# Kernel optimization log

Measured on AMD Instinct MI355X. Metric: run time of the kernel, lower is better.

## Reference

```python
import jax, jax.numpy as jnp
import numpy as np

B, CIN, H, W = 128, 64, 32, 32
COUT, K, STRIDE, PAD = 64, 3, 1, 1
HO = (H + 2 * PAD - K) // STRIDE + 1
WO = (W + 2 * PAD - K) // STRIDE + 1


def setup_inputs() -> dict:
    key = jax.random.key(0)
    k1, k2 = jax.random.split(key)
    x = jax.random.normal(k1, (B, CIN, H, W), dtype=jnp.float32)
    # weight scaled like torch init: randn / sqrt(k*k*Cin) (orthogonal_ in torch just
    # re-orthogonalizes; scale here matches the fan-in normalization)
    weight = jax.random.normal(k2, (HO, WO, COUT, CIN, K, K), dtype=jnp.float32) / np.sqrt(K * K * CIN)
    bias = jnp.full((COUT, HO, WO), 0.5, dtype=jnp.float32)
    return {"x": x, "weight": weight, "bias": bias}


def reference(x, weight, bias):
    # pad spatial dims
    xp = jnp.pad(x, ((0, 0), (0, 0), (PAD, PAD), (PAD, PAD)))
    # gather row windows: [B, C, Ho, K, Wp]
    ri = (jnp.arange(HO) * STRIDE)[:, None] + jnp.arange(K)[None, :]  # [Ho, K]
    ci = (jnp.arange(WO) * STRIDE)[:, None] + jnp.arange(K)[None, :]  # [Wo, K]
    rows = xp[:, :, ri, :]           # [B, C, Ho, K, Wp]
    patches = rows[:, :, :, :, ci]   # [B, C, Ho, K, Wo, K]
    # per-location matmul: b c h p w q , h w d c p q -> b d h w
    out = jnp.einsum('bchpwq,hwdcpq->bdhw', patches, weight)
    return out + bias[None]
```

## Files before the change

kernel.cpp:

```cpp
#include <hip/hip_runtime.h>
#include <hip/hip_bf16.h>

#define KT 576

typedef __attribute__((ext_vector_type(8))) short  short8;
typedef __attribute__((ext_vector_type(4))) float  f32x4;

#define VMCNT(n) asm volatile("s_waitcnt vmcnt(" #n ")" ::: "memory")
#define SB() __builtin_amdgcn_sched_barrier(0)

__device__ __forceinline__ unsigned short f2bf(float f) {
  union { float f; unsigned int u; } v; v.f = f;
  return (unsigned short)((v.u + 0x7FFFu + ((v.u >> 16) & 1u)) >> 16);
}

__global__ __launch_bounds__(256) void xC2_kernel(const float* __restrict__ x,
                                                  unsigned short* __restrict__ xC2) {
  const int hp = blockIdx.x, bb = blockIdx.y, t = threadIdx.x;
  __shared__ unsigned short tile[32 * 1024];
  const bool interior = (hp >= 1 && hp <= 32);
  if (interior) {
#pragma unroll 4
    for (int i = 0; i < 32; ++i) {
      const int row = i * 32 + (t >> 3);
      const int bl = row >> 6, c = row & 63;
      const int k = t & 7;
      const float4 v = *(const float4*)(x + ((size_t)(bb * 16 + bl) * 64 + c) * 1024 +
                                        (hp - 1) * 32 + k * 4);
      const int base = (k * 4) * 1024 + (c >> 3) * 128 + bl * 8 + (c & 7);
      tile[base]        = f2bf(v.x);
      tile[base + 1024] = f2bf(v.y);
      tile[base + 2048] = f2bf(v.z);
      tile[base + 3072] = f2bf(v.w);
    }
  }
  __syncthreads();
  unsigned short* dst = xC2 + (size_t)hp * 278528 + (size_t)bb * 1024;
  const uint4 z = make_uint4(0u, 0u, 0u, 0u);
  for (int idx = t; idx < 34 * 128; idx += 256) {
    const int wp = idx >> 7, s = idx & 127;
    uint4 v = z;
    if (interior && wp >= 1 && wp <= 32) v = *(const uint4*)&tile[(wp - 1) * 1024 + s * 8];
    *(uint4*)(dst + (size_t)wp * 8192 + s * 8) = v;
  }
}

__global__ __launch_bounds__(256, 1) void lc_main(const float* __restrict__ Wt,
                                                  const float* __restrict__ bias,
                                                  const unsigned short* __restrict__ xC2,
                                                  float* __restrict__ out) {
  __shared__ unsigned short Wl[2][32 * KT];
  __shared__ float blds[128];

  const int bid = (int)blockIdx.x;
  const int swz = (bid & 7) * 64 + (bid >> 3);
  const int h = swz >> 4, rem = swz & 15, wq = rem >> 1, half = rem & 1;
  const int t = threadIdx.x, lane = t & 63, wv = t >> 6;
  const int l15 = lane & 15, lg = lane >> 4;

  if (t < 128)
    blds[t] = bias[(half * 32 + (t & 31)) * 1024 + h * 32 + wq * 4 + (t >> 5)];

  const unsigned short* xA = xC2 + (size_t)wv * 2048 + lg * 128 + l15 * 8;
  const int x7 = l15 & 7;
  const int wrow0 = l15 * KT;
  const int wrow1 = (16 + l15) * KT;

  f32x4 acc[4][2][2];
#pragma unroll
  for (int j = 0; j < 4; ++j)
#pragma unroll
    for (int bt = 0; bt < 2; ++bt)
#pragma unroll
      for (int dt = 0; dt < 2; ++dt) acc[j][bt][dt] = (f32x4){0.f, 0.f, 0.f, 0.f};

  short8 As0[3][3], As1[3][3];
  float4 wreg[18];

#define ISSUE_W(jj)                                                           \
  {                                                                           \
    const float* ws = Wt + (size_t)(h * 32 + wq * 4 + (jj)) * (64 * KT) +     \
                      (size_t)half * (32 * KT);                               \
    _Pragma("unroll")                                                         \
    for (int i = 0; i < 18; ++i) {                                            \
      const float4* p = (const float4*)ws + (i * 256 + t);                    \
      asm volatile("global_load_dwordx4 %0, %1, off" : "=v"(wreg[i]) : "v"(p)); \
    }                                                                         \
  }

#define ISSUE_A(K)                                                            \
  {                                                                           \
    _Pragma("unroll")                                                         \
    for (int s = 0; s < 3; ++s) {                                             \
      const int step = ((K) % 6) * 3 + s;                                     \
      const int pq = step >> 1, p = pq / 3, q = pq - p * 3;                   \
      const size_t off = (size_t)(h + p) * 278528 +                           \
                         (size_t)(wq * 4 + (K) / 6 + q) * 8192 + (step & 1) * 512; \
      const short8* p0 = (const short8*)(xA + off);                           \
      const short8* p1 = (const short8*)(xA + off + 1024);                    \
      asm volatile("global_load_dwordx4 %0, %1, off" : "=v"(As0[(K) % 3][s]) : "v"(p0)); \
      asm volatile("global_load_dwordx4 %0, %1, off" : "=v"(As1[(K) % 3][s]) : "v"(p1)); \
    }                                                                         \
  }

#define SCATTER(buf)                                                          \
  {                                                                           \
    _Pragma("unroll")                                                         \
    for (int i = 0; i < 18; ++i) {                                            \
      const int f = (i * 256 + t) * 4;                                        \
      const int d = (((unsigned)(f >> 6)) * 7282u) >> 16;                     \
      int kn = f - d * 576;                                                   \
      int c = ((unsigned)kn * 7282u) >> 16;                                   \
      int r = kn - c * 9;                                                     \
      const float vv[4] = {wreg[i].x, wreg[i].y, wreg[i].z, wreg[i].w};       \
      _Pragma("unroll")                                                       \
      for (int jx = 0; jx < 4; ++jx) {                                        \
        const int kp = r * 64 + c;                                            \
        const int slot = (kp >> 3) ^ (d & 7);                                 \
        Wl[buf][d * KT + slot * 8 + (kp & 7)] = f2bf(vv[jx]);                 \
        if (++r == 9) { r = 0; ++c; }                                         \
      }                                                                       \
    }                                                                         \
  }

#define STEP(jj, gg, NN)                                                      \
  {                                                                           \
    VMCNT(NN);                                                                \
    SB();                                                                     \
    _Pragma("unroll")                                                         \
    for (int s = 0; s < 3; ++s) {                                             \
      const int sb = ((gg) * 3 + s) * 4 + lg;                                 \
      const short8 b0 = *(const short8*)&Wl[(jj) & 1][wrow0 + ((sb ^ x7) << 3)]; \
      const short8 b1 = *(const short8*)&Wl[(jj) & 1][wrow1 + ((sb ^ x7) << 3)]; \
      acc[(jj)][0][0] = __builtin_amdgcn_mfma_f32_16x16x32_bf16(As0[((jj) * 6 + (gg)) % 3][s], b0, acc[(jj)][0][0], 0, 0, 0); \
      acc[(jj)][1][0] = __builtin_amdgcn_mfma_f32_16x16x32_bf16(As1[((jj) * 6 + (gg)) % 3][s], b0, acc[(jj)][1][0], 0, 0, 0); \
      acc[(jj)][0][1] = __builtin_amdgcn_mfma_f32_16x16x32_bf16(As0[((jj) * 6 + (gg)) % 3][s], b1, acc[(jj)][0][1], 0, 0, 0); \
      acc[(jj)][1][1] = __builtin_amdgcn_mfma_f32_16x16x32_bf16(As1[((jj) * 6 + (gg)) % 3][s], b1, acc[(jj)][1][1], 0, 0, 0); \
    }                                                                         \
  }

  ISSUE_W(0);
  ISSUE_A(0); ISSUE_A(1); ISSUE_A(2);
  VMCNT(18);
  SB();
  SCATTER(0);
  __syncthreads();

  ISSUE_W(1);
  STEP(0, 0, 30); ISSUE_A(3);
  STEP(0, 1, 30); ISSUE_A(4);
  STEP(0, 2, 30); ISSUE_A(5);
  STEP(0, 3, 12); ISSUE_A(6);
  STEP(0, 4, 12); ISSUE_A(7);
  STEP(0, 5, 12); ISSUE_A(8);
  SCATTER(1);
  __syncthreads();

  ISSUE_W(2);
  STEP(1, 0, 30); ISSUE_A(9);
  STEP(1, 1, 30); ISSUE_A(10);
  STEP(1, 2, 30); ISSUE_A(11);
  STEP(1, 3, 12); ISSUE_A(12);
  STEP(1, 4, 12); ISSUE_A(13);
  STEP(1, 5, 12); ISSUE_A(14);
  SCATTER(0);
  __syncthreads();

  ISSUE_W(3);
  STEP(2, 0, 30); ISSUE_A(15);
  STEP(2, 1, 30); ISSUE_A(16);
  STEP(2, 2, 30); ISSUE_A(17);
  STEP(2, 3, 12); ISSUE_A(18);
  STEP(2, 4, 12); ISSUE_A(19);
  STEP(2, 5, 12); ISSUE_A(20);
  SCATTER(1);
  __syncthreads();

  STEP(3, 0, 12); ISSUE_A(21);
  STEP(3, 1, 12); ISSUE_A(22);
  STEP(3, 2, 12); ISSUE_A(23);
  STEP(3, 3, 12);
  STEP(3, 4, 6);
  STEP(3, 5, 0);

#pragma unroll
  for (int dt = 0; dt < 2; ++dt) {
    const int dd = dt * 16 + l15;
    const int dg = half * 32 + dd;
    const float bv0 = blds[dd], bv1 = blds[32 + dd], bv2 = blds[64 + dd], bv3 = blds[96 + dd];
#pragma unroll
    for (int bt = 0; bt < 2; ++bt) {
#pragma unroll
      for (int i = 0; i < 4; ++i) {
        const int b = wv * 32 + bt * 16 + lg * 4 + i;
        float4 v;
        v.x = acc[0][bt][dt][i] + bv0;
        v.y = acc[1][bt][dt][i] + bv1;
        v.z = acc[2][bt][dt][i] + bv2;
        v.w = acc[3][bt][dt][i] + bv3;
        *(float4*)(out + (size_t)b * 65536 + (size_t)dg * 1024 + h * 32 + wq * 4) = v;
      }
    }
  }
}

extern "C" void kernel_launch(void* const* d_in, const int* in_sizes, int n_in,
                              void* d_out, int out_size, void* d_ws, size_t ws_size,
                              hipStream_t stream) {
  const float* x    = (const float*)d_in[0];
  const float* wt   = (const float*)d_in[1];
  const float* bias = (const float*)d_in[2];
  float* out        = (float*)d_out;
  unsigned short* xC2 = (unsigned short*)d_ws;

  xC2_kernel<<<dim3(34, 8), 256, 0, stream>>>(x, xC2);
  lc_main<<<512, 256, 0, stream>>>(wt, bias, xC2, out);
}
```

Measured before the change: 68.54 us.

## Merge output-channel halves into one 512-thread block and split weight staging

Each block now covers all 64 output channels with 8 waves instead of 32 channels with 4 waves. The grid halves from 512 to 256 blocks and weight LDS doubles. The two channel halves share the same activation tiles, which cuts redundant activation fetches. Weight prefetch and scatter are split into two 9-load halves interleaved with the MFMA steps, and wait counts are retuned. With 256 blocks on 256 CUs this risks different occupancy and more LDS pressure per block.

```diff
diff --git a/kernel.cpp b/kernel.cpp
--- a/kernel.cpp
+++ b/kernel.cpp
@@ -45,26 +45,27 @@
   }
 }
 
-__global__ __launch_bounds__(256, 1) void lc_main(const float* __restrict__ Wt,
+__global__ __launch_bounds__(512, 1) void lc_main(const float* __restrict__ Wt,
                                                   const float* __restrict__ bias,
                                                   const unsigned short* __restrict__ xC2,
                                                   float* __restrict__ out) {
-  __shared__ unsigned short Wl[2][32 * KT];
-  __shared__ float blds[128];
+  __shared__ unsigned short Wl[2][64 * KT];
+  __shared__ float blds[256];
 
   const int bid = (int)blockIdx.x;
-  const int swz = (bid & 7) * 64 + (bid >> 3);
-  const int h = swz >> 4, rem = swz & 15, wq = rem >> 1, half = rem & 1;
+  const int swz = (bid & 7) * 32 + (bid >> 3);
+  const int h = swz >> 3, wq = swz & 7;
   const int t = threadIdx.x, lane = t & 63, wv = t >> 6;
+  const int bw = wv & 3, dh = wv >> 2;
   const int l15 = lane & 15, lg = lane >> 4;
 
-  if (t < 128)
-    blds[t] = bias[(half * 32 + (t & 31)) * 1024 + h * 32 + wq * 4 + (t >> 5)];
-
-  const unsigned short* xA = xC2 + (size_t)wv * 2048 + lg * 128 + l15 * 8;
+  if (t < 256)
+    blds[t] = bias[(t & 63) * 1024 + h * 32 + wq * 4 + (t >> 6)];
+
+  const unsigned short* xA = xC2 + (size_t)bw * 2048 + lg * 128 + l15 * 8;
   const int x7 = l15 & 7;
-  const int wrow0 = l15 * KT;
-  const int wrow1 = (16 + l15) * KT;
+  const int wrow0 = (dh * 32 + l15) * KT;
+  const int wrow1 = (dh * 32 + 16 + l15) * KT;
 
   f32x4 acc[4][2][2];
 #pragma unroll
@@ -75,15 +76,15 @@
       for (int dt = 0; dt < 2; ++dt) acc[j][bt][dt] = (f32x4){0.f, 0.f, 0.f, 0.f};
 
   short8 As0[3][3], As1[3][3];
-  float4 wreg[18];
-
-#define ISSUE_W(jj)                                                           \
+  float4 wreg[9];
+
+#define ISSUE_W9(jj, hs)                                                      \
   {                                                                           \
     const float* ws = Wt + (size_t)(h * 32 + wq * 4 + (jj)) * (64 * KT) +     \
-                      (size_t)half * (32 * KT);                               \
-    _Pragma("unroll")                                                         \
-    for (int i = 0; i < 18; ++i) {                                            \
-      const float4* p = (const float4*)ws + (i * 256 + t);                    \
+                      (size_t)(hs) * (32 * KT);                               \
+    _Pragma("unroll")                                                         \
+    for (int i = 0; i < 9; ++i) {                                             \
+      const float4* p = (const float4*)ws + (i * 512 + t);                    \
       asm volatile("global_load_dwordx4 %0, %1, off" : "=v"(wreg[i]) : "v"(p)); \
     }                                                                         \
   }
@@ -103,30 +104,29 @@
     }                                                                         \
   }
 
-#define SCATTER(buf)                                                          \
-  {                                                                           \
-    _Pragma("unroll")                                                         \
-    for (int i = 0; i < 18; ++i) {                                            \
-      const int f = (i * 256 + t) * 4;                                        \
-      const int d = (((unsigned)(f >> 6)) * 7282u) >> 16;                     \
-      int kn = f - d * 576;                                                   \
+#define SCATTER9(buf, hs)                                                     \
+  {                                                                           \
+    _Pragma("unroll")                                                         \
+    for (int i = 0; i < 9; ++i) {                                             \
+      const int f = (i * 512 + t) * 4;                                        \
+      const int dl = (((unsigned)(f >> 6)) * 7282u) >> 16;                    \
+      int kn = f - dl * 576;                                                  \
       int c = ((unsigned)kn * 7282u) >> 16;                                   \
       int r = kn - c * 9;                                                     \
+      const int drow = (hs) * 32 + dl;                                        \
       const float vv[4] = {wreg[i].x, wreg[i].y, wreg[i].z, wreg[i].w};       \
       _Pragma("unroll")                                                       \
       for (int jx = 0; jx < 4; ++jx) {                                        \
         const int kp = r * 64 + c;                                            \
-        const int slot = (kp >> 3) ^ (d & 7);                                 \
-        Wl[buf][d * KT + slot * 8 + (kp & 7)] = f2bf(vv[jx]);                 \
+        const int slot = (kp >> 3) ^ (drow & 7);                              \
+        Wl[buf][drow * KT + slot * 8 + (kp & 7)] = f2bf(vv[jx]);              \
         if (++r == 9) { r = 0; ++c; }                                         \
       }                                                                       \
     }                                                                         \
   }
 
-#define STEP(jj, gg, NN)                                                      \
-  {                                                                           \
-    VMCNT(NN);                                                                \
-    SB();                                                                     \
+#define MFMAS(jj, gg)                                                         \
+  {                                                                           \
     _Pragma("unroll")                                                         \
     for (int s = 0; s < 3; ++s) {                                             \
       const int sb = ((gg) * 3 + s) * 4 + lg;                                 \
@@ -139,42 +139,31 @@
     }                                                                         \
   }
 
-  ISSUE_W(0);
-  ISSUE_A(0); ISSUE_A(1); ISSUE_A(2);
-  VMCNT(18);
-  SB();
-  SCATTER(0);
-  __syncthreads();
-
-  ISSUE_W(1);
-  STEP(0, 0, 30); ISSUE_A(3);
-  STEP(0, 1, 30); ISSUE_A(4);
-  STEP(0, 2, 30); ISSUE_A(5);
-  STEP(0, 3, 12); ISSUE_A(6);
-  STEP(0, 4, 12); ISSUE_A(7);
-  STEP(0, 5, 12); ISSUE_A(8);
-  SCATTER(1);
-  __syncthreads();
-
-  ISSUE_W(2);
-  STEP(1, 0, 30); ISSUE_A(9);
-  STEP(1, 1, 30); ISSUE_A(10);
-  STEP(1, 2, 30); ISSUE_A(11);
-  STEP(1, 3, 12); ISSUE_A(12);
-  STEP(1, 4, 12); ISSUE_A(13);
-  STEP(1, 5, 12); ISSUE_A(14);
-  SCATTER(0);
-  __syncthreads();
-
-  ISSUE_W(3);
-  STEP(2, 0, 30); ISSUE_A(15);
-  STEP(2, 1, 30); ISSUE_A(16);
-  STEP(2, 2, 30); ISSUE_A(17);
-  STEP(2, 3, 12); ISSUE_A(18);
-  STEP(2, 4, 12); ISSUE_A(19);
-  STEP(2, 5, 12); ISSUE_A(20);
-  SCATTER(1);
-  __syncthreads();
+#define STEP(jj, gg, NN) { VMCNT(NN); SB(); MFMAS(jj, gg) }
+
+#define PHASE(jj)                                                             \
+  ISSUE_W9(jj + 1, 0);                                                        \
+  STEP(jj, 0, 21); ISSUE_A(6 * (jj) + 3);                                     \
+  STEP(jj, 1, 21); ISSUE_A(6 * (jj) + 4);                                     \
+  STEP(jj, 2, 21); ISSUE_A(6 * (jj) + 5);                                     \
+  STEP(jj, 3, 12); SCATTER9((jj + 1) & 1, 0); ISSUE_W9(jj + 1, 1);            \
+                   ISSUE_A(6 * (jj) + 6);                                     \
+  STEP(jj, 4, 21); ISSUE_A(6 * (jj) + 7);                                     \
+  STEP(jj, 5, 21); ISSUE_A(6 * (jj) + 8);                                     \
+  VMCNT(18); SB(); SCATTER9((jj + 1) & 1, 1);                                 \
+  __syncthreads(); SB();
+
+  ISSUE_W9(0, 0);
+  ISSUE_A(0);
+  VMCNT(6);  SB(); SCATTER9(0, 0);
+  ISSUE_W9(0, 1);
+  ISSUE_A(1); ISSUE_A(2);
+  VMCNT(12); SB(); SCATTER9(0, 1);
+  __syncthreads(); SB();
+
+  PHASE(0)
+  PHASE(1)
+  PHASE(2)
 
   STEP(3, 0, 12); ISSUE_A(21);
   STEP(3, 1, 12); ISSUE_A(22);
@@ -185,14 +174,13 @@
 
 #pragma unroll
   for (int dt = 0; dt < 2; ++dt) {
-    const int dd = dt * 16 + l15;
-    const int dg = half * 32 + dd;
-    const float bv0 = blds[dd], bv1 = blds[32 + dd], bv2 = blds[64 + dd], bv3 = blds[96 + dd];
+    const int dg = dh * 32 + dt * 16 + l15;
+    const float bv0 = blds[dg], bv1 = blds[64 + dg], bv2 = blds[128 + dg], bv3 = blds[192 + dg];
 #pragma unroll
     for (int bt = 0; bt < 2; ++bt) {
 #pragma unroll
       for (int i = 0; i < 4; ++i) {
-        const int b = wv * 32 + bt * 16 + lg * 4 + i;
+        const int b = bw * 32 + bt * 16 + lg * 4 + i;
         float4 v;
         v.x = acc[0][bt][dt][i] + bv0;
         v.y = acc[1][bt][dt][i] + bv1;
@@ -214,5 +202,5 @@
   unsigned short* xC2 = (unsigned short*)d_ws;
 
   xC2_kernel<<<dim3(34, 8), 256, 0, stream>>>(x, xC2);
-  lc_main<<<512, 256, 0, stream>>>(wt, bias, xC2, out);
-}
+  lc_main<<<256, 512, 0, stream>>>(wt, bias, xC2, out);
+}
```

Result: slower. 195.4 us (+185.0%).
